# Kernel optimization log

Hardware: AMD Instinct MI355X
Metric: run time of the kernel (lower is better)

The kernel has to match this reference:

```python
import jax, jax.numpy as jnp
import numpy as np

N_HEAD = 16
D_MODEL = 1024
D_HEAD = D_MODEL // N_HEAD
B, T = 2, 2048


def setup_inputs() -> dict:
    key = jax.random.key(0)
    k1, k2, k3 = jax.random.split(key, 3)
    x = jax.random.normal(k1, (B, T, D_MODEL), dtype=jnp.float32)
    w_attn = jax.random.normal(k2, (3 * D_MODEL, D_MODEL), dtype=jnp.float32) * (D_MODEL ** -0.5)
    w_proj = jax.random.normal(k3, (D_MODEL, D_MODEL), dtype=jnp.float32) * (D_MODEL ** -0.5)
    return {"x": x, "w_attn": w_attn, "w_proj": w_proj}


def _rms_norm(x):
    eps = jnp.asarray(jnp.finfo(x.dtype).eps, x.dtype)
    var = jnp.mean(jnp.square(x), axis=-1, keepdims=True)
    return x * jax.lax.rsqrt(var + eps)


def _rotate_half(x):
    x1, x2 = jnp.split(x, 2, axis=-1)
    return jnp.concatenate((-x2, x1), axis=-1)


def reference(x, w_attn, w_proj):
    Bx, Tx, C = x.shape
    qkv = jnp.einsum('btc,fc->btf', x, w_attn)  # [B,T,3C]
    q, k, v = jnp.split(qkv, 3, axis=-1)
    # [B, H, T, Dh]
    q = q.reshape(Bx, Tx, N_HEAD, D_HEAD).transpose(0, 2, 1, 3)
    k = k.reshape(Bx, Tx, N_HEAD, D_HEAD).transpose(0, 2, 1, 3)
    v = v.reshape(Bx, Tx, N_HEAD, D_HEAD).transpose(0, 2, 1, 3)
    # QK RMSNorm (no learned weight)
    q = _rms_norm(q)
    k = _rms_norm(k)
    # Rotary embedding over full d_head: freqs tiled twice
    inv_freq = 1.0 / (10000.0 ** (jnp.arange(0, D_HEAD, 2, dtype=jnp.float32) / D_HEAD))
    t = jnp.arange(Tx, dtype=jnp.float32)
    freqs = jnp.einsum('i,j->ij', t, inv_freq)  # [T, Dh/2]
    emb = jnp.concatenate((freqs, freqs), axis=-1)  # [T, Dh]
    cos = jnp.cos(emb)[None, None, :, :]
    sin = jnp.sin(emb)[None, None, :, :]
    q = q * cos + _rotate_half(q) * sin
    k = k * cos + _rotate_half(k) * sin
    # Causal SDPA
    scale = D_HEAD ** -0.5
    scores = jnp.einsum('bhqd,bhkd->bhqk', q, k) * scale
    causal = jnp.tril(jnp.ones((Tx, Tx), dtype=bool))
    scores = jnp.where(causal[None, None], scores, jnp.asarray(-jnp.inf, scores.dtype))
    attn = jax.nn.softmax(scores, axis=-1)
    y = jnp.einsum('bhqk,bhkd->bhqd', attn, v)
    y = y.transpose(0, 2, 1, 3).reshape(Bx, Tx, C)
    return jnp.einsum('btc,oc->bto', y, w_proj)
```

## Files before the change

kernel.cpp:

```cpp
#include <hip/hip_runtime.h>
#include <cstdint>
#include <cstddef>


typedef short bf16x8 __attribute__((ext_vector_type(8)));
typedef float floatx4 __attribute__((ext_vector_type(4)));
typedef unsigned short ushortx8 __attribute__((ext_vector_type(8)));
typedef unsigned short ushortx4 __attribute__((ext_vector_type(4)));
typedef unsigned int uintx2 __attribute__((ext_vector_type(2)));

#define DEVI __device__ __forceinline__

DEVI float bf2f(unsigned short u) {
    unsigned int x = ((unsigned int)u) << 16;
    return __builtin_bit_cast(float, x);
}
DEVI unsigned short f2bf(float f) {
    unsigned int u = __builtin_bit_cast(unsigned int, f);
    u += 0x7fffu + ((u >> 16) & 1u);
    return (unsigned short)(u >> 16);
}
DEVI unsigned int pkbf2(float a, float b) {
    unsigned int ua = __builtin_bit_cast(unsigned int, a) + 0x8000u;
    unsigned int ub = __builtin_bit_cast(unsigned int, b) + 0x8000u;
    return __builtin_amdgcn_perm(ub, ua, 0x07060302);
}

DEVI void glds16(const unsigned short* g, unsigned short* l) {
    __builtin_amdgcn_global_load_lds(
        (const __attribute__((address_space(1))) unsigned int*)g,
        (__attribute__((address_space(3))) unsigned int*)l, 16, 0, 0);
}

DEVI void cast8(unsigned short* dst, const float* src) {
    floatx4 a = *(const floatx4*)src;
    floatx4 b = *(const floatx4*)(src + 4);
    ushortx8 o;
    o[0] = f2bf(a[0]); o[1] = f2bf(a[1]); o[2] = f2bf(a[2]); o[3] = f2bf(a[3]);
    o[4] = f2bf(b[0]); o[5] = f2bf(b[1]); o[6] = f2bf(b[2]); o[7] = f2bf(b[3]);
    *(ushortx8*)dst = o;
}

__global__ __launch_bounds__(256)
void cast_inputs(const float* __restrict__ x, const float* __restrict__ wa,
                 const float* __restrict__ wp,
                 unsigned short* __restrict__ xb, unsigned short* __restrict__ wab,
                 unsigned short* __restrict__ wpb)
{
    size_t g = (size_t)blockIdx.x * 256 + threadIdx.x;
    size_t stride = (size_t)gridDim.x * 256;
    for (size_t i = g; i < (4194304 / 8); i += stride) cast8(xb  + i * 8, x  + i * 8);
    for (size_t i = g; i < (3145728 / 8); i += stride) cast8(wab + i * 8, wa + i * 8);
    for (size_t i = g; i < (1048576 / 8); i += stride) cast8(wpb + i * 8, wp + i * 8);
}

template <bool QKV_SPLIT, int BN, int BK>
__global__ __launch_bounds__(256)
void gemm_bt(const unsigned short* __restrict__ A, const unsigned short* __restrict__ B,
             unsigned short* __restrict__ Cqk, float* __restrict__ Cf,
             unsigned short* __restrict__ Vt, int M, int N, int K)
{
    constexpr int WCOLS = (BN == 128) ? 2 : 1;
    constexpr int WROWS = 4 / WCOLS;
    constexpr int MI    = 128 / (16 * WROWS);
    constexpr int LPR   = BK / 8;
    constexpr int RPI   = 64 / LPR;

    __shared__ __align__(16) unsigned short As[128 * BK];
    __shared__ __align__(16) unsigned short Bs[BN * BK];

    const int tid  = threadIdx.x;
    const int lane = tid & 63;
    const int w    = tid >> 6;
    const int wm   = w / WCOLS, wn = w % WCOLS;
    const int quad = lane >> 4;
    const int lm   = lane & 15;
    const int m0 = blockIdx.y * 128;
    const int n0 = blockIdx.x * BN;
    const int sr = lane / LPR;
    const int sc = (lane % LPR) * 8;

    floatx4 acc[MI][4] = {};

    for (int k0 = 0; k0 < K; k0 += BK) {
        __syncthreads();
        #pragma unroll
        for (int i = 0; i < 32 / RPI; ++i) {
            int r = w * 32 + i * RPI;
            glds16(&A[(size_t)(m0 + r + sr) * K + k0 + sc], &As[r * BK]);
        }
        #pragma unroll
        for (int i = 0; i < (BN / 4) / RPI; ++i) {
            int r = w * (BN / 4) + i * RPI;
            glds16(&B[(size_t)(n0 + r + sr) * K + k0 + sc], &Bs[r * BK]);
        }
        __syncthreads();

        #pragma unroll
        for (int kk = 0; kk < BK / 32; ++kk) {
            bf16x8 a[MI];
            #pragma unroll
            for (int i = 0; i < MI; ++i)
                a[i] = *(const bf16x8*)&As[(wm * (16 * MI) + i * 16 + lm) * BK + kk * 32 + quad * 8];
            #pragma unroll
            for (int j = 0; j < 4; ++j) {
                bf16x8 b = *(const bf16x8*)&Bs[(wn * 64 + j * 16 + lm) * BK + kk * 32 + quad * 8];
                #pragma unroll
                for (int i = 0; i < MI; ++i)
                    acc[i][j] = __builtin_amdgcn_mfma_f32_16x16x32_bf16(a[i], b, acc[i][j], 0, 0, 0);
            }
        }
    }

    if constexpr (QKV_SPLIT) {
        const bool is_v = (n0 + wn * 64) >= 2048;
        if (!is_v) {
            float rn[MI][4];
            #pragma unroll
            for (int i = 0; i < MI; ++i)
                #pragma unroll
                for (int r = 0; r < 4; ++r) {
                    float s = 0.0f;
                    #pragma unroll
                    for (int j = 0; j < 4; ++j) s += acc[i][j][r] * acc[i][j][r];
                    s += __shfl_xor(s, 1, 64);
                    s += __shfl_xor(s, 2, 64);
                    s += __shfl_xor(s, 4, 64);
                    s += __shfl_xor(s, 8, 64);
                    rn[i][r] = rsqrtf(s * (1.0f / 64.0f) + 1.1920929e-07f);
                }
            float invf[4];
            #pragma unroll
            for (int j = 0; j < 4; ++j) {
                int d = j * 16 + lm;
                invf[j] = __expf(-(float)(d & 31) * 0.28782313662425572f);
            }
            #pragma unroll
            for (int i = 0; i < MI; ++i)
                #pragma unroll
                for (int r = 0; r < 4; ++r) {
                    int row = m0 + wm * (16 * MI) + i * 16 + quad * 4 + r;
                    float t = (float)(row & 2047);
                    float g = rn[i][r];
                    #pragma unroll
                    for (int j = 0; j < 4; ++j) {
                        int d = j * 16 + lm;
                        float sn, cs;
                        __sincosf(t * invf[j], &sn, &cs);
                        float v  = acc[i][j][r] * g;
                        float vp = acc[i][j ^ 2][r] * g;
                        float sgn = (d < 32) ? -1.0f : 1.0f;
                        Cqk[(size_t)row * 2048 + (n0 + wn * 64 + d)] =
                            f2bf(v * cs + sgn * vp * sn);
                    }
                }
        } else {
            #pragma unroll
            for (int i = 0; i < MI; ++i)
                #pragma unroll
                for (int j = 0; j < 4; ++j) {
                    int col  = n0 + wn * 64 + j * 16 + lm;
                    int row0 = m0 + wm * (16 * MI) + i * 16 + quad * 4;
                    int bq = row0 >> 11, t0 = row0 & 2047;
                    ushortx4 pk;
                    #pragma unroll
                    for (int r = 0; r < 4; ++r) pk[r] = f2bf(acc[i][j][r]);
                    *(ushortx4*)&Vt[((size_t)(bq * 1024 + (col - 2048))) * 2048 + t0] = pk;
                }
        }
    } else {
        #pragma unroll
        for (int i = 0; i < MI; ++i)
            #pragma unroll
            for (int j = 0; j < 4; ++j) {
                int col  = n0 + wn * 64 + j * 16 + lm;
                int row0 = m0 + wm * (16 * MI) + i * 16 + quad * 4;
                #pragma unroll
                for (int r = 0; r < 4; ++r)
                    Cf[(size_t)(row0 + r) * N + col] = acc[i][j][r];
            }
    }
}

__global__ __launch_bounds__(256)
void attention(const unsigned short* __restrict__ qk,
               const unsigned short* __restrict__ Vt,
               unsigned short* __restrict__ Y)
{
    constexpr int LD = 72;
    __shared__ __align__(16) unsigned short QPs[64 * LD];
    __shared__ __align__(16) unsigned short Ks [64 * LD];
    __shared__ __align__(16) unsigned short Vs [64 * LD];

    const int tid  = threadIdx.x;
    const int lane = tid & 63;
    const int w    = tid >> 6;
    const int quad = lane >> 4;
    const int lm   = lane & 15;

    const int bh = blockIdx.x;
    const int qt = 31 - blockIdx.y;
    const int b  = bh >> 4, h = bh & 15;
    const int q0 = qt * 64;
    const int qrow = q0 + w * 16 + lm;

    const int r0 = tid >> 3, r1 = r0 + 32, pc = (tid & 7) * 8;
    const unsigned short* kp0 = qk + (size_t)b * 2048 * 2048 + 1024 + h * 64
                              + (size_t)r0 * 2048 + pc;
    const unsigned short* kp1 = kp0 + (size_t)32 * 2048;
    const unsigned short* vp0 = Vt + (size_t)bh * 64 * 2048 + (size_t)r0 * 2048 + pc;
    const unsigned short* vp1 = vp0 + (size_t)32 * 2048;

    #pragma unroll
    for (int i = 0; i < 2; ++i) {
        int c = i * 256 + tid, row = c >> 3, col = (c & 7) * 8;
        *(ushortx8*)&QPs[row * LD + col] =
            *(const ushortx8*)&qk[((size_t)(b * 2048 + q0 + row)) * 2048 + h * 64 + col];
    }

    ushortx8 kreg0 = *(const ushortx8*)kp0, kreg1 = *(const ushortx8*)kp1;
    ushortx8 vreg0 = *(const ushortx8*)vp0, vreg1 = *(const ushortx8*)vp1;
    kp0 += (size_t)64 * 2048; kp1 += (size_t)64 * 2048;
    vp0 += 64; vp1 += 64;

    __syncthreads();
    bf16x8 qf[2];
    #pragma unroll
    for (int kk = 0; kk < 2; ++kk)
        qf[kk] = *(const bf16x8*)&QPs[(w * 16 + lm) * LD + kk * 32 + quad * 8];

    bf16x8 ones;
    #pragma unroll
    for (int i = 0; i < 8; ++i) ones[i] = (short)0x3F80;

    floatx4 o[4] = {};
    floatx4 l_acc = {};
    const float c1 = 0.125f * 1.44269504f;
    const float c2 = 8.0f   * 1.44269504f;

    for (int kt = 0; kt < qt; ++kt) {
        __syncthreads();
        *(ushortx8*)&Ks[r0 * LD + pc] = kreg0;
        *(ushortx8*)&Ks[r1 * LD + pc] = kreg1;
        *(ushortx8*)&Vs[r0 * LD + pc] = vreg0;
        *(ushortx8*)&Vs[r1 * LD + pc] = vreg1;
        __syncthreads();

        kreg0 = *(const ushortx8*)kp0; kreg1 = *(const ushortx8*)kp1;
        vreg0 = *(const ushortx8*)vp0; vreg1 = *(const ushortx8*)vp1;
        kp0 += (size_t)64 * 2048; kp1 += (size_t)64 * 2048;
        vp0 += 64; vp1 += 64;

        floatx4 sa[4] = {};
        #pragma unroll
        for (int kk = 0; kk < 2; ++kk)
            #pragma unroll
            for (int j = 0; j < 4; ++j) {
                bf16x8 kf = *(const bf16x8*)&Ks[(j * 16 + lm) * LD + kk * 32 + quad * 8];
                sa[j] = __builtin_amdgcn_mfma_f32_16x16x32_bf16(kf, qf[kk], sa[j], 0, 0, 0);
            }

        #pragma unroll
        for (int j = 0; j < 4; ++j) {
            float p0 = exp2f(sa[j][0] * c1 - c2);
            float p1 = exp2f(sa[j][1] * c1 - c2);
            float p2 = exp2f(sa[j][2] * c1 - c2);
            float p3 = exp2f(sa[j][3] * c1 - c2);
            uintx2 pk;
            pk[0] = pkbf2(p0, p1);
            pk[1] = pkbf2(p2, p3);
            *(uintx2*)&QPs[(w * 16 + lm) * LD + j * 16 + quad * 4] = pk;
        }

        #pragma unroll
        for (int kk = 0; kk < 2; ++kk) {
            bf16x8 pf = *(const bf16x8*)&QPs[(w * 16 + lm) * LD + kk * 32 + quad * 8];
            #pragma unroll
            for (int j = 0; j < 4; ++j) {
                bf16x8 vf = *(const bf16x8*)&Vs[(j * 16 + lm) * LD + kk * 32 + quad * 8];
                o[j] = __builtin_amdgcn_mfma_f32_16x16x32_bf16(pf, vf, o[j], 0, 0, 0);
            }
            l_acc = __builtin_amdgcn_mfma_f32_16x16x32_bf16(pf, ones, l_acc, 0, 0, 0);
        }
    }

    {
        __syncthreads();
        *(ushortx8*)&Ks[r0 * LD + pc] = kreg0;
        *(ushortx8*)&Ks[r1 * LD + pc] = kreg1;
        *(ushortx8*)&Vs[r0 * LD + pc] = vreg0;
        *(ushortx8*)&Vs[r1 * LD + pc] = vreg1;
        __syncthreads();

        floatx4 sa[4] = {};
        #pragma unroll
        for (int kk = 0; kk < 2; ++kk)
            #pragma unroll
            for (int j = 0; j < 4; ++j) {
                bf16x8 kf = *(const bf16x8*)&Ks[(j * 16 + lm) * LD + kk * 32 + quad * 8];
                sa[j] = __builtin_amdgcn_mfma_f32_16x16x32_bf16(kf, qf[kk], sa[j], 0, 0, 0);
            }

        #pragma unroll
        for (int j = 0; j < 4; ++j) {
            int kb = q0 + j * 16 + quad * 4;
            float p0 = (kb + 0 > qrow) ? 0.0f : exp2f(sa[j][0] * c1 - c2);
            float p1 = (kb + 1 > qrow) ? 0.0f : exp2f(sa[j][1] * c1 - c2);
            float p2 = (kb + 2 > qrow) ? 0.0f : exp2f(sa[j][2] * c1 - c2);
            float p3 = (kb + 3 > qrow) ? 0.0f : exp2f(sa[j][3] * c1 - c2);
            uintx2 pk;
            pk[0] = pkbf2(p0, p1);
            pk[1] = pkbf2(p2, p3);
            *(uintx2*)&QPs[(w * 16 + lm) * LD + j * 16 + quad * 4] = pk;
        }

        #pragma unroll
        for (int kk = 0; kk < 2; ++kk) {
            bf16x8 pf = *(const bf16x8*)&QPs[(w * 16 + lm) * LD + kk * 32 + quad * 8];
            #pragma unroll
            for (int j = 0; j < 4; ++j) {
                bf16x8 vf = *(const bf16x8*)&Vs[(j * 16 + lm) * LD + kk * 32 + quad * 8];
                o[j] = __builtin_amdgcn_mfma_f32_16x16x32_bf16(pf, vf, o[j], 0, 0, 0);
            }
            l_acc = __builtin_amdgcn_mfma_f32_16x16x32_bf16(pf, ones, l_acc, 0, 0, 0);
        }
    }

    float rinv[4];
    #pragma unroll
    for (int r = 0; r < 4; ++r) rinv[r] = 1.0f / l_acc[r];

    #pragma unroll
    for (int j = 0; j < 4; ++j) {
        int colg = h * 64 + j * 16 + lm;
        #pragma unroll
        for (int r = 0; r < 4; ++r) {
            int rowg = q0 + w * 16 + quad * 4 + r;
            Y[((size_t)(b * 2048 + rowg)) * 1024 + colg] = f2bf(o[j][r] * rinv[r]);
        }
    }
}

extern "C" void kernel_launch(void* const* d_in, const int* in_sizes, int n_in,
                              void* d_out, int out_size, void* d_ws, size_t ws_size,
                              hipStream_t stream)
{
    const float* x      = (const float*)d_in[0];
    const float* w_attn = (const float*)d_in[1];
    const float* w_proj = (const float*)d_in[2];
    float* out = (float*)d_out;

    unsigned short* qkbuf = (unsigned short*)d_ws;
    unsigned short* Vtb   = qkbuf + (size_t)4096 * 2048;
    unsigned short* y     = Vtb   + (size_t)32 * 64 * 2048;
    unsigned short* wpb   = y     + (size_t)4096 * 1024;
    unsigned short* xb  = (unsigned short*)d_out;
    unsigned short* wab = xb + (size_t)4096 * 1024;

    dim3 blk(256);
    cast_inputs<<<dim3(1024), blk, 0, stream>>>(x, w_attn, w_proj, xb, wab, wpb);
    gemm_bt<true, 128, 32>
        <<<dim3(24, 32), blk, 0, stream>>>(xb, wab, qkbuf, nullptr, Vtb, 4096, 3072, 1024);
    attention<<<dim3(32, 32), blk, 0, stream>>>(qkbuf, Vtb, y);
    gemm_bt<false, 64, 64>
        <<<dim3(16, 32), blk, 0, stream>>>(y, wpb, nullptr, out, nullptr, 4096, 1024, 1024);
}
```

Measured before the change: 184.1 us.

## Double-buffer K/V tiles in LDS to use one barrier per iteration

Splits the K and V shared-memory tiles into two ping-pong buffers so the next tile is stored while the current one is consumed. This removes one of the two block-wide barriers per kv tile and lets LDS stores overlap with MFMA work. The loop is unrolled by two via a macro, and the diagonal tile is handled in the final step. The trade-off is extra LDS use per block, which may reduce occupancy.

```diff
diff --git a/kernel.cpp b/kernel.cpp
--- a/kernel.cpp
+++ b/kernel.cpp
@@ -182,6 +182,59 @@
     }
 }
 
+#define ATTN_STEP(KSc, VSc, KSn, VSn, KT, DG, LAST)                            \
+  do {                                                                         \
+    if (!(LAST)) {                                                             \
+      *(ushortx8*)&(KSn)[r0 * LD + pc] = kreg0;                                \
+      *(ushortx8*)&(KSn)[r1 * LD + pc] = kreg1;                                \
+      *(ushortx8*)&(VSn)[r0 * LD + pc] = vreg0;                                \
+      *(ushortx8*)&(VSn)[r1 * LD + pc] = vreg1;                                \
+      if ((KT) + 2 <= qt) {                                                    \
+        kreg0 = *(const ushortx8*)kp0; kreg1 = *(const ushortx8*)kp1;          \
+        vreg0 = *(const ushortx8*)vp0; vreg1 = *(const ushortx8*)vp1;          \
+        kp0 += (size_t)64 * 2048; kp1 += (size_t)64 * 2048;                    \
+        vp0 += 64; vp1 += 64;                                                  \
+      }                                                                        \
+    }                                                                          \
+    floatx4 sa[4] = {};                                                        \
+    _Pragma("unroll")                                                          \
+    for (int kk = 0; kk < 2; ++kk)                                             \
+      _Pragma("unroll")                                                        \
+      for (int j = 0; j < 4; ++j) {                                            \
+        bf16x8 kf = *(const bf16x8*)&(KSc)[(j * 16 + lm) * LD + kk * 32 + quad * 8]; \
+        sa[j] = __builtin_amdgcn_mfma_f32_16x16x32_bf16(kf, qf[kk], sa[j], 0, 0, 0); \
+      }                                                                        \
+    _Pragma("unroll")                                                          \
+    for (int j = 0; j < 4; ++j) {                                              \
+      float p0 = exp2f(sa[j][0] * c1 - c2);                                    \
+      float p1 = exp2f(sa[j][1] * c1 - c2);                                    \
+      float p2 = exp2f(sa[j][2] * c1 - c2);                                    \
+      float p3 = exp2f(sa[j][3] * c1 - c2);                                    \
+      if (DG) {                                                                \
+        int kb = (KT) * 64 + j * 16 + quad * 4;                                \
+        if (kb + 0 > qrow) p0 = 0.0f;                                          \
+        if (kb + 1 > qrow) p1 = 0.0f;                                          \
+        if (kb + 2 > qrow) p2 = 0.0f;                                          \
+        if (kb + 3 > qrow) p3 = 0.0f;                                          \
+      }                                                                        \
+      uintx2 pk;                                                               \
+      pk[0] = pkbf2(p0, p1);                                                   \
+      pk[1] = pkbf2(p2, p3);                                                   \
+      *(uintx2*)&QPs[(w * 16 + lm) * LD + j * 16 + quad * 4] = pk;             \
+    }                                                                          \
+    _Pragma("unroll")                                                          \
+    for (int kk = 0; kk < 2; ++kk) {                                           \
+      bf16x8 pf = *(const bf16x8*)&QPs[(w * 16 + lm) * LD + kk * 32 + quad * 8]; \
+      _Pragma("unroll")                                                        \
+      for (int j = 0; j < 4; ++j) {                                            \
+        bf16x8 vf = *(const bf16x8*)&(VSc)[(j * 16 + lm) * LD + kk * 32 + quad * 8]; \
+        o[j] = __builtin_amdgcn_mfma_f32_16x16x32_bf16(pf, vf, o[j], 0, 0, 0); \
+      }                                                                        \
+      l_acc = __builtin_amdgcn_mfma_f32_16x16x32_bf16(pf, ones, l_acc, 0, 0, 0); \
+    }                                                                          \
+    if (!(LAST)) __syncthreads();                                              \
+  } while (0)
+
 __global__ __launch_bounds__(256)
 void attention(const unsigned short* __restrict__ qk,
                const unsigned short* __restrict__ Vt,
@@ -189,8 +242,10 @@
 {
     constexpr int LD = 72;
     __shared__ __align__(16) unsigned short QPs[64 * LD];
-    __shared__ __align__(16) unsigned short Ks [64 * LD];
-    __shared__ __align__(16) unsigned short Vs [64 * LD];
+    __shared__ __align__(16) unsigned short Ks0[64 * LD];
+    __shared__ __align__(16) unsigned short Ks1[64 * LD];
+    __shared__ __align__(16) unsigned short Vs0[64 * LD];
+    __shared__ __align__(16) unsigned short Vs1[64 * LD];
 
     const int tid  = threadIdx.x;
     const int lane = tid & 63;
@@ -222,8 +277,18 @@
     ushortx8 vreg0 = *(const ushortx8*)vp0, vreg1 = *(const ushortx8*)vp1;
     kp0 += (size_t)64 * 2048; kp1 += (size_t)64 * 2048;
     vp0 += 64; vp1 += 64;
-
+    *(ushortx8*)&Ks0[r0 * LD + pc] = kreg0;
+    *(ushortx8*)&Ks0[r1 * LD + pc] = kreg1;
+    *(ushortx8*)&Vs0[r0 * LD + pc] = vreg0;
+    *(ushortx8*)&Vs0[r1 * LD + pc] = vreg1;
+    if (qt >= 1) {
+        kreg0 = *(const ushortx8*)kp0; kreg1 = *(const ushortx8*)kp1;
+        vreg0 = *(const ushortx8*)vp0; vreg1 = *(const ushortx8*)vp1;
+        kp0 += (size_t)64 * 2048; kp1 += (size_t)64 * 2048;
+        vp0 += 64; vp1 += 64;
+    }
     __syncthreads();
+
     bf16x8 qf[2];
     #pragma unroll
     for (int kk = 0; kk < 2; ++kk)
@@ -238,92 +303,16 @@
     const float c1 = 0.125f * 1.44269504f;
     const float c2 = 8.0f   * 1.44269504f;
 
-    for (int kt = 0; kt < qt; ++kt) {
-        __syncthreads();
-        *(ushortx8*)&Ks[r0 * LD + pc] = kreg0;
-        *(ushortx8*)&Ks[r1 * LD + pc] = kreg1;
-        *(ushortx8*)&Vs[r0 * LD + pc] = vreg0;
-        *(ushortx8*)&Vs[r1 * LD + pc] = vreg1;
-        __syncthreads();
-
-        kreg0 = *(const ushortx8*)kp0; kreg1 = *(const ushortx8*)kp1;
-        vreg0 = *(const ushortx8*)vp0; vreg1 = *(const ushortx8*)vp1;
-        kp0 += (size_t)64 * 2048; kp1 += (size_t)64 * 2048;
-        vp0 += 64; vp1 += 64;
-
-        floatx4 sa[4] = {};
-        #pragma unroll
-        for (int kk = 0; kk < 2; ++kk)
-            #pragma unroll
-            for (int j = 0; j < 4; ++j) {
-                bf16x8 kf = *(const bf16x8*)&Ks[(j * 16 + lm) * LD + kk * 32 + quad * 8];
-                sa[j] = __builtin_amdgcn_mfma_f32_16x16x32_bf16(kf, qf[kk], sa[j], 0, 0, 0);
-            }
-
-        #pragma unroll
-        for (int j = 0; j < 4; ++j) {
-            float p0 = exp2f(sa[j][0] * c1 - c2);
-            float p1 = exp2f(sa[j][1] * c1 - c2);
-            float p2 = exp2f(sa[j][2] * c1 - c2);
-            float p3 = exp2f(sa[j][3] * c1 - c2);
-            uintx2 pk;
-            pk[0] = pkbf2(p0, p1);
-            pk[1] = pkbf2(p2, p3);
-            *(uintx2*)&QPs[(w * 16 + lm) * LD + j * 16 + quad * 4] = pk;
-        }
-
-        #pragma unroll
-        for (int kk = 0; kk < 2; ++kk) {
-            bf16x8 pf = *(const bf16x8*)&QPs[(w * 16 + lm) * LD + kk * 32 + quad * 8];
-            #pragma unroll
-            for (int j = 0; j < 4; ++j) {
-                bf16x8 vf = *(const bf16x8*)&Vs[(j * 16 + lm) * LD + kk * 32 + quad * 8];
-                o[j] = __builtin_amdgcn_mfma_f32_16x16x32_bf16(pf, vf, o[j], 0, 0, 0);
-            }
-            l_acc = __builtin_amdgcn_mfma_f32_16x16x32_bf16(pf, ones, l_acc, 0, 0, 0);
-        }
-    }
-
-    {
-        __syncthreads();
-        *(ushortx8*)&Ks[r0 * LD + pc] = kreg0;
-        *(ushortx8*)&Ks[r1 * LD + pc] = kreg1;
-        *(ushortx8*)&Vs[r0 * LD + pc] = vreg0;
-        *(ushortx8*)&Vs[r1 * LD + pc] = vreg1;
-        __syncthreads();
-
-        floatx4 sa[4] = {};
-        #pragma unroll
-        for (int kk = 0; kk < 2; ++kk)
-            #pragma unroll
-            for (int j = 0; j < 4; ++j) {
-                bf16x8 kf = *(const bf16x8*)&Ks[(j * 16 + lm) * LD + kk * 32 + quad * 8];
-                sa[j] = __builtin_amdgcn_mfma_f32_16x16x32_bf16(kf, qf[kk], sa[j], 0, 0, 0);
-            }
-
-        #pragma unroll
-        for (int j = 0; j < 4; ++j) {
-            int kb = q0 + j * 16 + quad * 4;
-            float p0 = (kb + 0 > qrow) ? 0.0f : exp2f(sa[j][0] * c1 - c2);
-            float p1 = (kb + 1 > qrow) ? 0.0f : exp2f(sa[j][1] * c1 - c2);
-            float p2 = (kb + 2 > qrow) ? 0.0f : exp2f(sa[j][2] * c1 - c2);
-            float p3 = (kb + 3 > qrow) ? 0.0f : exp2f(sa[j][3] * c1 - c2);
-            uintx2 pk;
-            pk[0] = pkbf2(p0, p1);
-            pk[1] = pkbf2(p2, p3);
-            *(uintx2*)&QPs[(w * 16 + lm) * LD + j * 16 + quad * 4] = pk;
-        }
-
-        #pragma unroll
-        for (int kk = 0; kk < 2; ++kk) {
-            bf16x8 pf = *(const bf16x8*)&QPs[(w * 16 + lm) * LD + kk * 32 + quad * 8];
-            #pragma unroll
-            for (int j = 0; j < 4; ++j) {
-                bf16x8 vf = *(const bf16x8*)&Vs[(j * 16 + lm) * LD + kk * 32 + quad * 8];
-                o[j] = __builtin_amdgcn_mfma_f32_16x16x32_bf16(pf, vf, o[j], 0, 0, 0);
-            }
-            l_acc = __builtin_amdgcn_mfma_f32_16x16x32_bf16(pf, ones, l_acc, 0, 0, 0);
-        }
+    int kt = 0;
+    for (; kt + 1 < qt; kt += 2) {
+        ATTN_STEP(Ks0, Vs0, Ks1, Vs1, kt,     false, false);
+        ATTN_STEP(Ks1, Vs1, Ks0, Vs0, kt + 1, false, false);
+    }
+    if (kt < qt) {
+        ATTN_STEP(Ks0, Vs0, Ks1, Vs1, kt, false, false);
+        ATTN_STEP(Ks1, Vs1, Ks0, Vs0, qt, true, true);
+    } else {
+        ATTN_STEP(Ks0, Vs0, Ks1, Vs1, qt, true, true);
     }
 
     float rinv[4];
```

After: 180.4 us. -2.0%, faster.
